# Optimization experiments

Measured on AMD Instinct MI355X. Metric: run time of the kernel, lower is better.

Reference implementation:

```python
import jax, jax.numpy as jnp
import numpy as np
from jax import lax

# Geometry constants (stand-in for beijing* globals)
A = 96           # beijingAngleNum
P = 4            # beijingPlanes
DET0, DET1 = 256, 8   # beijingSubDetectorSize [u, v]
NZ, NY, NX = 32, 256, 256  # beijingVolumeSize (nz = P * DET1)
T = 256          # ray integration steps
LAMB = 0.01


def _bilinear(vol, ix, iy):
    # vol: [nz, ny, nx]; ix, iy: [...] index-space coords. Zero outside.
    nz, ny, nx = vol.shape
    x0 = jnp.floor(ix); y0 = jnp.floor(iy)
    fx = (ix - x0).astype(vol.dtype); fy = (iy - y0).astype(vol.dtype)
    x0i = x0.astype(jnp.int32); y0i = y0.astype(jnp.int32)

    def g(yi, xi):
        valid = ((xi >= 0) & (xi < nx) & (yi >= 0) & (yi < ny)).astype(vol.dtype)
        v = vol[:, jnp.clip(yi, 0, ny - 1), jnp.clip(xi, 0, nx - 1)]  # [nz, ...]
        return v * valid

    return (g(y0i, x0i) * (1 - fy) * (1 - fx)
            + g(y0i, x0i + 1) * (1 - fy) * fx
            + g(y0i + 1, x0i) * fy * (1 - fx)
            + g(y0i + 1, x0i + 1) * fy * fx)


def forward_project(vol):
    # vol: [NZ, NY, NX] -> sinogram [A, NZ, DET0], parallel-beam over 180 deg
    angles = jnp.arange(A, dtype=jnp.float32) * (np.pi / A)
    u = jnp.arange(DET0, dtype=jnp.float32) - (DET0 - 1) / 2.0  # detector coord
    t = jnp.arange(T, dtype=jnp.float32) - (T - 1) / 2.0        # along-ray coord

    def per_angle(_, th):
        c, s = jnp.cos(th), jnp.sin(th)
        x = -u[:, None] * s + t[None, :] * c   # [DET0, T]
        y = u[:, None] * c + t[None, :] * s
        samp = _bilinear(vol, x + (NX - 1) / 2.0, y + (NY - 1) / 2.0)  # [NZ,DET0,T]
        return None, samp.sum(-1)  # line integral, [NZ, DET0]

    _, S = lax.scan(per_angle, None, angles)
    return S  # [A, NZ, DET0]


def back_project(S):
    # S: [A, NZ, DET0] -> volume [NZ, NY, NX] (adjoint-style backprojection)
    angles = jnp.arange(A, dtype=jnp.float32) * (np.pi / A)
    yy = jnp.arange(NY, dtype=jnp.float32) - (NY - 1) / 2.0
    xx = jnp.arange(NX, dtype=jnp.float32) - (NX - 1) / 2.0
    Y, X = jnp.meshgrid(yy, xx, indexing='ij')  # [NY, NX]

    def per_angle(acc, inp):
        th, Sa = inp  # Sa: [NZ, DET0]
        c, s = jnp.cos(th), jnp.sin(th)
        ub = -X * s + Y * c + (DET0 - 1) / 2.0  # detector bin coord [NY,NX]
        u0 = jnp.floor(ub)
        fu = (ub - u0).astype(Sa.dtype)
        u0i = u0.astype(jnp.int32)

        def g(ui):
            valid = ((ui >= 0) & (ui < DET0)).astype(Sa.dtype)
            return Sa[:, jnp.clip(ui, 0, DET0 - 1)] * valid  # [NZ,NY,NX]

        val = g(u0i) * (1 - fu) + g(u0i + 1) * fu
        return acc + val, None

    vol0 = jnp.zeros((NZ, NY, NX), dtype=S.dtype)
    vol, _ = lax.scan(per_angle, vol0, (angles, S))
    return vol


def setup_inputs() -> dict:
    key = jax.random.key(0)
    k1, k2 = jax.random.split(key)
    x = jax.random.normal(k1, (1, 1, NZ, NY, NX), dtype=jnp.float32)
    p = jax.random.normal(k2, (1, 1, A * P, DET1, DET0), dtype=jnp.float32)
    return {"x": x, "p": p}


def reference(x, p):
    vol = x[0, 0]                              # [NZ, NY, NX]
    S = forward_project(vol)                   # [A, NZ, DET0] native
    # ForwardProjection wrapper: (A,P,V,U) -> permute -> flat external layout
    ext = S.reshape(A, P, DET1, DET0).transpose(0, 2, 1, 3).reshape(1, 1, A * P, DET1, DET0)
    residual = ext - p
    # BackProjection wrapper: undo external layout back to native
    res_native = residual.reshape(A, DET1, P, DET0).transpose(0, 2, 1, 3).reshape(A, NZ, DET0)
    volb = back_project(res_native)            # [NZ, NY, NX]
    return (-LAMB * volb)[None, None]          # [1,1,NZ,NY,NX]
```

## Files before the change

kernel.cpp:

```cpp
#include <hip/hip_runtime.h>

#define A     96
#define DET0  256
#define NZ    32
#define NY    256
#define NX    256
#define T     256
#define LAMB  0.01f

#define TRIG_OFF  0
#define REST_OFF  256
#define VOLB_OFF  786688
#define PART_OFF  1835264
#define RES_ELEMS 786432

__device__ __forceinline__ unsigned short f2bf_rne(float f) {
    unsigned u = __float_as_uint(f);
    unsigned r = u + 0x7FFF + ((u >> 16) & 1);
    return (unsigned short)(r >> 16);
}
__device__ __forceinline__ float blo(unsigned u) { return __uint_as_float(u << 16); }
__device__ __forceinline__ float bhi(unsigned u) { return __uint_as_float(u & 0xFFFF0000u); }

__device__ __forceinline__ void acc8(float* acc, uint4 q, float w) {
    acc[0] = fmaf(w, blo(q.x), acc[0]); acc[1] = fmaf(w, bhi(q.x), acc[1]);
    acc[2] = fmaf(w, blo(q.y), acc[2]); acc[3] = fmaf(w, bhi(q.y), acc[3]);
    acc[4] = fmaf(w, blo(q.z), acc[4]); acc[5] = fmaf(w, bhi(q.z), acc[5]);
    acc[6] = fmaf(w, blo(q.w), acc[6]); acc[7] = fmaf(w, bhi(q.w), acc[7]);
}

__global__ __launch_bounds__(256) void k_transpose(const float* __restrict__ src,
                                                   unsigned short* __restrict__ vol_b,
                                                   float* __restrict__ trig) {
    __shared__ float lds[64 * 33];
    const int y   = blockIdx.y;
    const int x0  = blockIdx.x * 64;
    const int tid = threadIdx.x;

    if (blockIdx.x == 0 && y == 0 && tid < A) {
        float th = (float)tid * (float)(3.14159265358979323846 / (double)A);
        trig[2 * tid]     = cosf(th);
        trig[2 * tid + 1] = sinf(th);
    }

    const int xr = tid & 63;
    const int zr = tid >> 6;
    #pragma unroll
    for (int pz = 0; pz < 8; ++pz) {
        int z = pz * 4 + zr;
        lds[xr * 33 + z] = src[(z * NY + y) * NX + x0 + xr];
    }
    __syncthreads();
    const int zw = tid & 31;
    const int xw = tid >> 5;
    #pragma unroll
    for (int px = 0; px < 8; ++px) {
        int xi = px * 8 + xw;
        vol_b[(y * NX + x0 + xi) * NZ + zw] = f2bf_rne(lds[xi * 33 + zw]);
    }
}

__device__ __forceinline__ void rng(float g, float b, float L, float H,
                                    float& lo, float& hi) {
    if (fabsf(g) > 1e-5f) {
        float r0 = (L - b) / g, r1 = (H - b) / g;
        lo = fminf(r0, r1); hi = fmaxf(r0, r1);
    } else {
        bool in = (b >= L && b <= H);
        lo = in ? -1e9f : 1e9f;
        hi = in ? 1e9f : -1e9f;
    }
}
__device__ __forceinline__ int clampi(float v) {
    return (int)fminf(fmaxf(v, -2.f), 258.f);
}

__device__ __forceinline__ void sample_edge(const char* base, float ix, float iy,
                                            float* acc) {
    float xf = floorf(ix), yf = floorf(iy);
    float fx = ix - xf, fy = iy - yf;
    int x0 = (int)xf, y0 = (int)yf;
    float wx0 = 1.f - fx, wx1 = fx, wy0 = 1.f - fy, wy1 = fy;
    if ((unsigned)x0 >= NX)       wx0 = 0.f;
    if ((unsigned)(x0 + 1) >= NX) wx1 = 0.f;
    if ((unsigned)y0 >= NY)       wy0 = 0.f;
    if ((unsigned)(y0 + 1) >= NY) wy1 = 0.f;
    if ((wx0 == 0.f && wx1 == 0.f) || (wy0 == 0.f && wy1 == 0.f)) return;
    int cx0 = min(max(x0, 0), NX - 1);
    int cx1 = min(max(x0 + 1, 0), NX - 1);
    int cy0 = min(max(y0, 0), NY - 1);
    int cy1 = min(max(y0 + 1, 0), NY - 1);
    uint4 q00 = *(const uint4*)(base + ((size_t)((cy0 << 8) + cx0) << 6));
    uint4 q01 = *(const uint4*)(base + ((size_t)((cy0 << 8) + cx1) << 6));
    uint4 q10 = *(const uint4*)(base + ((size_t)((cy1 << 8) + cx0) << 6));
    uint4 q11 = *(const uint4*)(base + ((size_t)((cy1 << 8) + cx1) << 6));
    acc8(acc, q00, wy0 * wx0);
    acc8(acc, q01, wy0 * wx1);
    acc8(acc, q10, wy1 * wx0);
    acc8(acc, q11, wy1 * wx1);
}

__global__ __launch_bounds__(256) void k_forward(const unsigned short* __restrict__ vol_b,
                                                 const float* __restrict__ trig,
                                                 float* __restrict__ part,
                                                 int tlen) {
    const int tid = threadIdx.x;
    const int a  = blockIdx.z;
    const int u  = blockIdx.x * 64 + (tid >> 2);
    const int zq = tid & 3;
    const int t0 = blockIdx.y * tlen;

    const float c = trig[2 * a];
    const float s = trig[2 * a + 1];
    const float uu = (float)u - 127.5f;
    const float bx = fmaf(-uu, s, 127.5f);
    const float by = fmaf(uu, c, 127.5f);

    float lo1, hi1, lo2, hi2;
    rng(c, bx, -1.f, 256.f, lo1, hi1);
    rng(s, by, -1.f, 256.f, lo2, hi2);
    float fl = fmaxf(lo1, lo2), fh = fminf(hi1, hi2);
    int tF0 = max(t0, clampi(ceilf(fl + 127.5f)));
    int tF1 = min(t0 + tlen - 1, clampi(floorf(fh + 127.5f)));
    rng(c, bx, 1.f, 253.5f, lo1, hi1);
    rng(s, by, 1.f, 253.5f, lo2, hi2);
    float il = fmaxf(lo1, lo2), ih = fminf(hi1, hi2);
    int tI0 = max(clampi(ceilf(il + 127.5f)) + 1, tF0);
    int tI1 = min(clampi(floorf(ih + 127.5f)) - 1, tF1);
    if (tI0 > tI1) { tI0 = tF1 + 1; tI1 = tF1; }

    const char* base = (const char*)vol_b + zq * 16;
    float acc[8];
    #pragma unroll
    for (int k = 0; k < 8; ++k) acc[k] = 0.f;

    for (int t = tF0; t < tI0; ++t) {
        float ttf = (float)t - 127.5f;
        sample_edge(base, fmaf(ttf, c, bx), fmaf(ttf, s, by), acc);
    }
    for (int t = tI0; t <= tI1; ++t) {
        float ttf = (float)t - 127.5f;
        float ix = fmaf(ttf, c, bx);
        float iy = fmaf(ttf, s, by);
        float xf = floorf(ix), yf = floorf(iy);
        float fx = ix - xf, fy = iy - yf;
        int row = ((int)yf << 8) + (int)xf;
        const char* p0 = base + ((size_t)row << 6);
        uint4 q00 = *(const uint4*)(p0);
        uint4 q01 = *(const uint4*)(p0 + 64);
        uint4 q10 = *(const uint4*)(p0 + 16384);
        uint4 q11 = *(const uint4*)(p0 + 16384 + 64);
        float wx0 = 1.f - fx, wy0 = 1.f - fy;
        acc8(acc, q00, wy0 * wx0);
        acc8(acc, q01, wy0 * fx);
        acc8(acc, q10, fy * wx0);
        acc8(acc, q11, fy * fx);
    }
    for (int t = tI1 + 1; t <= tF1; ++t) {
        float ttf = (float)t - 127.5f;
        sample_edge(base, fmaf(ttf, c, bx), fmaf(ttf, s, by), acc);
    }

    float4* dst = (float4*)(part + (size_t)blockIdx.y * RES_ELEMS +
                            ((a * DET0 + u) * NZ + zq * 8));
    dst[0] = make_float4(acc[0], acc[1], acc[2], acc[3]);
    dst[1] = make_float4(acc[4], acc[5], acc[6], acc[7]);
}

__global__ __launch_bounds__(256) void k_combine(const float* __restrict__ p,
                                                 const float* __restrict__ part,
                                                 float* __restrict__ res_t,
                                                 int C) {
    __shared__ float lds[256 * 33];
    const int a = blockIdx.x;
    const int u = threadIdx.x;
    #pragma unroll
    for (int z = 0; z < 32; ++z) {
        int pidx = a * 8192 + (((z & 7) << 2) + (z >> 3)) * 256 + u;
        lds[u * 33 + z] = p[pidx];
    }
    __syncthreads();
    #pragma unroll
    for (int k = 0; k < 8; ++k) {
        int j4 = k * 256 + threadIdx.x;
        int j  = j4 * 4;
        int uu = j >> 5;
        int zb = j & 31;
        float4 v = make_float4(-lds[uu * 33 + zb],     -lds[uu * 33 + zb + 1],
                               -lds[uu * 33 + zb + 2], -lds[uu * 33 + zb + 3]);
        for (int c = 0; c < C; ++c) {
            float4 w = ((const float4*)(part + (size_t)c * RES_ELEMS))[a * 2048 + j4];
            v.x += w.x; v.y += w.y; v.z += w.z; v.w += w.w;
        }
        ((float4*)res_t)[a * 2048 + j4] = v;
    }
}

__global__ __launch_bounds__(256) void k_backward(const float* __restrict__ res_t,
                                                  const float* __restrict__ trig,
                                                  float* __restrict__ out) {
    __shared__ float4 wb[A * 32];
    __shared__ float  ob[32 * 33];
    const int tid = threadIdx.x;
    const int y  = blockIdx.y;
    const int xb = blockIdx.x * 32;

    for (int e = tid; e < A * 32; e += 256) {
        int a  = e >> 5;
        int xs = e & 31;
        float cc = trig[2 * a];
        float ss = trig[2 * a + 1];
        float xx = (float)(xb + xs) - 127.5f;
        float yy = (float)y - 127.5f;
        float ub = fmaf(-xx, ss, fmaf(yy, cc, 127.5f));
        float uf = floorf(ub);
        float fu = ub - uf;
        int i0 = (int)uf;
        float w0 = ((unsigned)i0 < DET0) ? (1.f - fu) : 0.f;
        float w1 = ((unsigned)(i0 + 1) < DET0) ? fu : 0.f;
        int c0 = min(max(i0, 0), DET0 - 1);
        int c1 = min(max(i0 + 1, 0), DET0 - 1);
        wb[e] = make_float4(w0, w1,
                            __int_as_float(((a * DET0 + c0) * NZ) << 2),
                            __int_as_float(((a * DET0 + c1) * NZ) << 2));
    }
    __syncthreads();

    const int xs = tid >> 3;
    const int zq = tid & 7;
    const char* rbase = (const char*)res_t + zq * 16;
    float4 acc = make_float4(0.f, 0.f, 0.f, 0.f);
    #pragma unroll 4
    for (int a = 0; a < A; ++a) {
        float4 e = wb[a * 32 + xs];
        float4 v0 = *(const float4*)(rbase + __float_as_int(e.z));
        float4 v1 = *(const float4*)(rbase + __float_as_int(e.w));
        acc.x = fmaf(e.x, v0.x, fmaf(e.y, v1.x, acc.x));
        acc.y = fmaf(e.x, v0.y, fmaf(e.y, v1.y, acc.y));
        acc.z = fmaf(e.x, v0.z, fmaf(e.y, v1.z, acc.z));
        acc.w = fmaf(e.x, v0.w, fmaf(e.y, v1.w, acc.w));
    }

    ob[(zq * 4 + 0) * 33 + xs] = acc.x;
    ob[(zq * 4 + 1) * 33 + xs] = acc.y;
    ob[(zq * 4 + 2) * 33 + xs] = acc.z;
    ob[(zq * 4 + 3) * 33 + xs] = acc.w;
    __syncthreads();

    const int z  = tid >> 3;
    const int x4 = (tid & 7) * 4;
    float4 o = make_float4(ob[z * 33 + x4],     ob[z * 33 + x4 + 1],
                           ob[z * 33 + x4 + 2], ob[z * 33 + x4 + 3]);
    float4* dst = (float4*)(out + (size_t)z * (NY * NX) + y * NX + xb + x4);
    *dst = make_float4(-LAMB * o.x, -LAMB * o.y, -LAMB * o.z, -LAMB * o.w);
}

extern "C" void kernel_launch(void* const* d_in, const int* in_sizes, int n_in,
                              void* d_out, int out_size, void* d_ws, size_t ws_size,
                              hipStream_t stream) {
    const float* x = (const float*)d_in[0];
    const float* p = (const float*)d_in[1];
    float* out = (float*)d_out;
    float* ws  = (float*)d_ws;

    float*          trig  = ws + TRIG_OFF;
    float*          res_t = ws + REST_OFF;
    unsigned short* vol_b = (unsigned short*)(ws + VOLB_OFF);
    float*          part  = ws + PART_OFF;

    size_t avail = ws_size / 4;
    int C = 8;
    while (C > 1 && (size_t)PART_OFF + (size_t)C * RES_ELEMS > avail) C >>= 1;
    int tlen = T / C;

    k_transpose<<<dim3(NX / 64, NY), 256, 0, stream>>>(x, vol_b, trig);
    k_forward  <<<dim3(4, C, A), 256, 0, stream>>>(vol_b, trig, part, tlen);
    k_combine  <<<dim3(A), 256, 0, stream>>>(p, part, res_t, C);
    k_backward <<<dim3(NX / 32, NY), 256, 0, stream>>>(res_t, trig, out);
}
```

Before: 205.4 us.

## Use fp32 volume, balance forward ray chunks, register-block backprojection rows

The forward volume copy is now stored in fp32 instead of bf16. This drops the bf16 rounding but doubles the bytes each bilinear gather reads. The forward kernel cuts rays into 32-step windows paired from both ends, spreads them over 4 partials to balance load, and uses a 1D grid ordered by angle with launch_bounds(256,4). The combine kernel runs on more blocks, and the backward kernel drops the LDS weight table in favour of computing weights inline, with each thread now covering 4 y rows to reuse trig and cut launch overhead.

```diff
diff --git a/kernel.cpp b/kernel.cpp
--- a/kernel.cpp
+++ b/kernel.cpp
@@ -10,27 +10,12 @@
 
 #define TRIG_OFF  0
 #define REST_OFF  256
-#define VOLB_OFF  786688
-#define PART_OFF  1835264
+#define VOLT_OFF  786688
+#define PART_OFF  2883840
 #define RES_ELEMS 786432
 
-__device__ __forceinline__ unsigned short f2bf_rne(float f) {
-    unsigned u = __float_as_uint(f);
-    unsigned r = u + 0x7FFF + ((u >> 16) & 1);
-    return (unsigned short)(r >> 16);
-}
-__device__ __forceinline__ float blo(unsigned u) { return __uint_as_float(u << 16); }
-__device__ __forceinline__ float bhi(unsigned u) { return __uint_as_float(u & 0xFFFF0000u); }
-
-__device__ __forceinline__ void acc8(float* acc, uint4 q, float w) {
-    acc[0] = fmaf(w, blo(q.x), acc[0]); acc[1] = fmaf(w, bhi(q.x), acc[1]);
-    acc[2] = fmaf(w, blo(q.y), acc[2]); acc[3] = fmaf(w, bhi(q.y), acc[3]);
-    acc[4] = fmaf(w, blo(q.z), acc[4]); acc[5] = fmaf(w, bhi(q.z), acc[5]);
-    acc[6] = fmaf(w, blo(q.w), acc[6]); acc[7] = fmaf(w, bhi(q.w), acc[7]);
-}
-
 __global__ __launch_bounds__(256) void k_transpose(const float* __restrict__ src,
-                                                   unsigned short* __restrict__ vol_b,
+                                                   float* __restrict__ vol_t,
                                                    float* __restrict__ trig) {
     __shared__ float lds[64 * 33];
     const int y   = blockIdx.y;
@@ -56,8 +41,15 @@
     #pragma unroll
     for (int px = 0; px < 8; ++px) {
         int xi = px * 8 + xw;
-        vol_b[(y * NX + x0 + xi) * NZ + zw] = f2bf_rne(lds[xi * 33 + zw]);
-    }
+        vol_t[(size_t)(y * NX + x0 + xi) * NZ + zw] = lds[xi * 33 + zw];
+    }
+}
+
+__device__ __forceinline__ void acc8f(float* acc, float4 qa, float4 qb, float w) {
+    acc[0] = fmaf(w, qa.x, acc[0]); acc[1] = fmaf(w, qa.y, acc[1]);
+    acc[2] = fmaf(w, qa.z, acc[2]); acc[3] = fmaf(w, qa.w, acc[3]);
+    acc[4] = fmaf(w, qb.x, acc[4]); acc[5] = fmaf(w, qb.y, acc[5]);
+    acc[6] = fmaf(w, qb.z, acc[6]); acc[7] = fmaf(w, qb.w, acc[7]);
 }
 
 __device__ __forceinline__ void rng(float g, float b, float L, float H,
@@ -90,25 +82,28 @@
     int cx1 = min(max(x0 + 1, 0), NX - 1);
     int cy0 = min(max(y0, 0), NY - 1);
     int cy1 = min(max(y0 + 1, 0), NY - 1);
-    uint4 q00 = *(const uint4*)(base + ((size_t)((cy0 << 8) + cx0) << 6));
-    uint4 q01 = *(const uint4*)(base + ((size_t)((cy0 << 8) + cx1) << 6));
-    uint4 q10 = *(const uint4*)(base + ((size_t)((cy1 << 8) + cx0) << 6));
-    uint4 q11 = *(const uint4*)(base + ((size_t)((cy1 << 8) + cx1) << 6));
-    acc8(acc, q00, wy0 * wx0);
-    acc8(acc, q01, wy0 * wx1);
-    acc8(acc, q10, wy1 * wx0);
-    acc8(acc, q11, wy1 * wx1);
-}
-
-__global__ __launch_bounds__(256) void k_forward(const unsigned short* __restrict__ vol_b,
-                                                 const float* __restrict__ trig,
-                                                 float* __restrict__ part,
-                                                 int tlen) {
-    const int tid = threadIdx.x;
-    const int a  = blockIdx.z;
-    const int u  = blockIdx.x * 64 + (tid >> 2);
+    const char* p00 = base + ((size_t)((cy0 << 8) + cx0) << 7);
+    const char* p01 = base + ((size_t)((cy0 << 8) + cx1) << 7);
+    const char* p10 = base + ((size_t)((cy1 << 8) + cx0) << 7);
+    const char* p11 = base + ((size_t)((cy1 << 8) + cx1) << 7);
+    acc8f(acc, *(const float4*)p00, *(const float4*)(p00 + 16), wy0 * wx0);
+    acc8f(acc, *(const float4*)p01, *(const float4*)(p01 + 16), wy0 * wx1);
+    acc8f(acc, *(const float4*)p10, *(const float4*)(p10 + 16), wy1 * wx0);
+    acc8f(acc, *(const float4*)p11, *(const float4*)(p11 + 16), wy1 * wx1);
+}
+
+__global__ __launch_bounds__(256, 4) void k_forward(const float* __restrict__ vol_t,
+                                                    const float* __restrict__ trig,
+                                                    float* __restrict__ part,
+                                                    int P) {
+    const unsigned bid = blockIdx.x;
+    const unsigned a   = bid % (unsigned)A;
+    const unsigned r   = bid / (unsigned)A;
+    const unsigned pr  = r % (unsigned)P;
+    const unsigned ug  = r / (unsigned)P;
+    const int tid = threadIdx.x;
+    const int u  = ug * 64 + (tid >> 2);
     const int zq = tid & 3;
-    const int t0 = blockIdx.y * tlen;
 
     const float c = trig[2 * a];
     const float s = trig[2 * a + 1];
@@ -120,49 +115,64 @@
     rng(c, bx, -1.f, 256.f, lo1, hi1);
     rng(s, by, -1.f, 256.f, lo2, hi2);
     float fl = fmaxf(lo1, lo2), fh = fminf(hi1, hi2);
-    int tF0 = max(t0, clampi(ceilf(fl + 127.5f)));
-    int tF1 = min(t0 + tlen - 1, clampi(floorf(fh + 127.5f)));
+    const int gF0 = clampi(ceilf(fl + 127.5f));
+    const int gF1 = clampi(floorf(fh + 127.5f));
     rng(c, bx, 1.f, 253.5f, lo1, hi1);
     rng(s, by, 1.f, 253.5f, lo2, hi2);
     float il = fmaxf(lo1, lo2), ih = fminf(hi1, hi2);
-    int tI0 = max(clampi(ceilf(il + 127.5f)) + 1, tF0);
-    int tI1 = min(clampi(floorf(ih + 127.5f)) - 1, tF1);
-    if (tI0 > tI1) { tI0 = tF1 + 1; tI1 = tF1; }
-
-    const char* base = (const char*)vol_b + zq * 16;
+    const int gI0 = clampi(ceilf(il + 127.5f)) + 1;
+    const int gI1 = clampi(floorf(ih + 127.5f)) - 1;
+
+    const char* base = (const char*)vol_t + zq * 32;
     float acc[8];
     #pragma unroll
     for (int k = 0; k < 8; ++k) acc[k] = 0.f;
 
-    for (int t = tF0; t < tI0; ++t) {
-        float ttf = (float)t - 127.5f;
-        sample_edge(base, fmaf(ttf, c, bx), fmaf(ttf, s, by), acc);
-    }
-    for (int t = tI0; t <= tI1; ++t) {
-        float ttf = (float)t - 127.5f;
-        float ix = fmaf(ttf, c, bx);
-        float iy = fmaf(ttf, s, by);
-        float xf = floorf(ix), yf = floorf(iy);
-        float fx = ix - xf, fy = iy - yf;
-        int row = ((int)yf << 8) + (int)xf;
-        const char* p0 = base + ((size_t)row << 6);
-        uint4 q00 = *(const uint4*)(p0);
-        uint4 q01 = *(const uint4*)(p0 + 64);
-        uint4 q10 = *(const uint4*)(p0 + 16384);
-        uint4 q11 = *(const uint4*)(p0 + 16384 + 64);
-        float wx0 = 1.f - fx, wy0 = 1.f - fy;
-        acc8(acc, q00, wy0 * wx0);
-        acc8(acc, q01, wy0 * fx);
-        acc8(acc, q10, fy * wx0);
-        acc8(acc, q11, fy * fx);
-    }
-    for (int t = tI1 + 1; t <= tF1; ++t) {
-        float ttf = (float)t - 127.5f;
-        sample_edge(base, fmaf(ttf, c, bx), fmaf(ttf, s, by), acc);
-    }
-
-    float4* dst = (float4*)(part + (size_t)blockIdx.y * RES_ELEMS +
-                            ((a * DET0 + u) * NZ + zq * 8));
+    for (int wi = (int)pr; wi < 4; wi += P) {
+        #pragma unroll
+        for (int side = 0; side < 2; ++side) {
+            int w = side ? (7 - wi) : wi;
+            int tF0 = max(w * 32, gF0);
+            int tF1 = min(w * 32 + 31, gF1);
+            int tI0 = max(gI0, tF0);
+            int tI1 = min(gI1, tF1);
+            if (tI0 > tI1) { tI0 = tF1 + 1; tI1 = tF1; }
+
+            for (int t = tF0; t < tI0; ++t) {
+                float ttf = (float)t - 127.5f;
+                sample_edge(base, fmaf(ttf, c, bx), fmaf(ttf, s, by), acc);
+            }
+            for (int t = tI0; t <= tI1; ++t) {
+                float ttf = (float)t - 127.5f;
+                float ix = fmaf(ttf, c, bx);
+                float iy = fmaf(ttf, s, by);
+                float xf = floorf(ix), yf = floorf(iy);
+                float fx = ix - xf, fy = iy - yf;
+                int row = ((int)yf << 8) + (int)xf;
+                const char* p0 = base + ((size_t)row << 7);
+                float4 a00 = *(const float4*)(p0);
+                float4 b00 = *(const float4*)(p0 + 16);
+                float4 a01 = *(const float4*)(p0 + 128);
+                float4 b01 = *(const float4*)(p0 + 144);
+                float4 a10 = *(const float4*)(p0 + 32768);
+                float4 b10 = *(const float4*)(p0 + 32784);
+                float4 a11 = *(const float4*)(p0 + 32896);
+                float4 b11 = *(const float4*)(p0 + 32912);
+                float wx0 = 1.f - fx, wy0 = 1.f - fy;
+                acc8f(acc, a00, b00, wy0 * wx0);
+                acc8f(acc, a01, b01, wy0 * fx);
+                acc8f(acc, a10, b10, fy * wx0);
+                acc8f(acc, a11, b11, fy * fx);
+            }
+            for (int t = tI1 + 1; t <= tF1; ++t) {
+                float ttf = (float)t - 127.5f;
+                sample_edge(base, fmaf(ttf, c, bx), fmaf(ttf, s, by), acc);
+            }
+        }
+    }
+
+    float4* dst = (float4*)(part + (size_t)pr * RES_ELEMS +
+                            (((int)a * DET0 + u) * NZ + zq * 8));
     dst[0] = make_float4(acc[0], acc[1], acc[2], acc[3]);
     dst[1] = make_float4(acc[4], acc[5], acc[6], acc[7]);
 }
@@ -170,89 +180,92 @@
 __global__ __launch_bounds__(256) void k_combine(const float* __restrict__ p,
                                                  const float* __restrict__ part,
                                                  float* __restrict__ res_t,
-                                                 int C) {
-    __shared__ float lds[256 * 33];
-    const int a = blockIdx.x;
-    const int u = threadIdx.x;
-    #pragma unroll
-    for (int z = 0; z < 32; ++z) {
-        int pidx = a * 8192 + (((z & 7) << 2) + (z >> 3)) * 256 + u;
-        lds[u * 33 + z] = p[pidx];
+                                                 int P) {
+    __shared__ float lds[64 * 33];
+    const int a  = blockIdx.x;
+    const int uq = blockIdx.y;
+    const int tid = threadIdx.x;
+    #pragma unroll
+    for (int k = 0; k < 8; ++k) {
+        int e  = k * 256 + tid;
+        int uo = e & 63;
+        int z  = e >> 6;
+        int pidx = a * 8192 + (((z & 7) << 2) + (z >> 3)) * 256 + uq * 64 + uo;
+        lds[uo * 33 + z] = p[pidx];
     }
     __syncthreads();
     #pragma unroll
-    for (int k = 0; k < 8; ++k) {
-        int j4 = k * 256 + threadIdx.x;
-        int j  = j4 * 4;
-        int uu = j >> 5;
-        int zb = j & 31;
-        float4 v = make_float4(-lds[uu * 33 + zb],     -lds[uu * 33 + zb + 1],
-                               -lds[uu * 33 + zb + 2], -lds[uu * 33 + zb + 3]);
-        for (int c = 0; c < C; ++c) {
-            float4 w = ((const float4*)(part + (size_t)c * RES_ELEMS))[a * 2048 + j4];
+    for (int k = 0; k < 2; ++k) {
+        int j4 = k * 256 + tid;
+        int uo = j4 >> 3;
+        int zb = (j4 & 7) * 4;
+        float4 v = make_float4(-lds[uo * 33 + zb],     -lds[uo * 33 + zb + 1],
+                               -lds[uo * 33 + zb + 2], -lds[uo * 33 + zb + 3]);
+        size_t gi = (size_t)a * 2048 + uq * 512 + j4;
+        for (int c = 0; c < P; ++c) {
+            float4 w = ((const float4*)(part + (size_t)c * RES_ELEMS))[gi];
             v.x += w.x; v.y += w.y; v.z += w.z; v.w += w.w;
         }
-        ((float4*)res_t)[a * 2048 + j4] = v;
+        ((float4*)res_t)[gi] = v;
     }
 }
 
 __global__ __launch_bounds__(256) void k_backward(const float* __restrict__ res_t,
                                                   const float* __restrict__ trig,
                                                   float* __restrict__ out) {
-    __shared__ float4 wb[A * 32];
-    __shared__ float  ob[32 * 33];
-    const int tid = threadIdx.x;
-    const int y  = blockIdx.y;
+    __shared__ float ob[32 * 33];
+    const int tid = threadIdx.x;
+    const int xs = tid >> 3;
+    const int zq = tid & 7;
     const int xb = blockIdx.x * 32;
-
-    for (int e = tid; e < A * 32; e += 256) {
-        int a  = e >> 5;
-        int xs = e & 31;
+    const int yb = blockIdx.y * 4;
+    const float xx = (float)(xb + xs) - 127.5f;
+    const float yy = (float)yb - 127.5f;
+
+    float4 acc[4];
+    #pragma unroll
+    for (int k = 0; k < 4; ++k) acc[k] = make_float4(0.f, 0.f, 0.f, 0.f);
+
+    const char* rbase = (const char*)res_t + zq * 16;
+    for (int a = 0; a < A; ++a) {
         float cc = trig[2 * a];
         float ss = trig[2 * a + 1];
-        float xx = (float)(xb + xs) - 127.5f;
-        float yy = (float)y - 127.5f;
         float ub = fmaf(-xx, ss, fmaf(yy, cc, 127.5f));
-        float uf = floorf(ub);
-        float fu = ub - uf;
-        int i0 = (int)uf;
-        float w0 = ((unsigned)i0 < DET0) ? (1.f - fu) : 0.f;
-        float w1 = ((unsigned)(i0 + 1) < DET0) ? fu : 0.f;
-        int c0 = min(max(i0, 0), DET0 - 1);
-        int c1 = min(max(i0 + 1, 0), DET0 - 1);
-        wb[e] = make_float4(w0, w1,
-                            __int_as_float(((a * DET0 + c0) * NZ) << 2),
-                            __int_as_float(((a * DET0 + c1) * NZ) << 2));
-    }
-    __syncthreads();
-
-    const int xs = tid >> 3;
-    const int zq = tid & 7;
-    const char* rbase = (const char*)res_t + zq * 16;
-    float4 acc = make_float4(0.f, 0.f, 0.f, 0.f);
-    #pragma unroll 4
-    for (int a = 0; a < A; ++a) {
-        float4 e = wb[a * 32 + xs];
-        float4 v0 = *(const float4*)(rbase + __float_as_int(e.z));
-        float4 v1 = *(const float4*)(rbase + __float_as_int(e.w));
-        acc.x = fmaf(e.x, v0.x, fmaf(e.y, v1.x, acc.x));
-        acc.y = fmaf(e.x, v0.y, fmaf(e.y, v1.y, acc.y));
-        acc.z = fmaf(e.x, v0.z, fmaf(e.y, v1.z, acc.z));
-        acc.w = fmaf(e.x, v0.w, fmaf(e.y, v1.w, acc.w));
-    }
-
-    ob[(zq * 4 + 0) * 33 + xs] = acc.x;
-    ob[(zq * 4 + 1) * 33 + xs] = acc.y;
-    ob[(zq * 4 + 2) * 33 + xs] = acc.z;
-    ob[(zq * 4 + 3) * 33 + xs] = acc.w;
-    __syncthreads();
-
-    const int z  = tid >> 3;
-    const int x4 = (tid & 7) * 4;
-    float4 o = make_float4(ob[z * 33 + x4],     ob[z * 33 + x4 + 1],
-                           ob[z * 33 + x4 + 2], ob[z * 33 + x4 + 3]);
-    float4* dst = (float4*)(out + (size_t)z * (NY * NX) + y * NX + xb + x4);
-    *dst = make_float4(-LAMB * o.x, -LAMB * o.y, -LAMB * o.z, -LAMB * o.w);
+        int abase = a * DET0;
+        #pragma unroll
+        for (int y = 0; y < 4; ++y) {
+            float uf = floorf(ub);
+            float fu = ub - uf;
+            int i0 = (int)uf;
+            float w0 = ((unsigned)i0 < 256u) ? (1.f - fu) : 0.f;
+            float w1 = ((unsigned)(i0 + 1) < 256u) ? fu : 0.f;
+            int c0 = min(max(i0, 0), 255);
+            int c1 = min(max(i0 + 1, 0), 255);
+            float4 v0 = *(const float4*)(rbase + ((size_t)(abase + c0) << 7));
+            float4 v1 = *(const float4*)(rbase + ((size_t)(abase + c1) << 7));
+            acc[y].x = fmaf(w0, v0.x, fmaf(w1, v1.x, acc[y].x));
+            acc[y].y = fmaf(w0, v0.y, fmaf(w1, v1.y, acc[y].y));
+            acc[y].z = fmaf(w0, v0.z, fmaf(w1, v1.z, acc[y].z));
+            acc[y].w = fmaf(w0, v0.w, fmaf(w1, v1.w, acc[y].w));
+            ub += cc;
+        }
+    }
+
+    #pragma unroll
+    for (int y = 0; y < 4; ++y) {
+        __syncthreads();
+        ob[(zq * 4 + 0) * 33 + xs] = acc[y].x;
+        ob[(zq * 4 + 1) * 33 + xs] = acc[y].y;
+        ob[(zq * 4 + 2) * 33 + xs] = acc[y].z;
+        ob[(zq * 4 + 3) * 33 + xs] = acc[y].w;
+        __syncthreads();
+        int z  = tid >> 3;
+        int x4 = (tid & 7) * 4;
+        float4 o = make_float4(ob[z * 33 + x4],     ob[z * 33 + x4 + 1],
+                               ob[z * 33 + x4 + 2], ob[z * 33 + x4 + 3]);
+        *(float4*)(out + (size_t)z * (NY * NX) + (yb + y) * NX + xb + x4) =
+            make_float4(-LAMB * o.x, -LAMB * o.y, -LAMB * o.z, -LAMB * o.w);
+    }
 }
 
 extern "C" void kernel_launch(void* const* d_in, const int* in_sizes, int n_in,
@@ -263,18 +276,17 @@
     float* out = (float*)d_out;
     float* ws  = (float*)d_ws;
 
-    float*          trig  = ws + TRIG_OFF;
-    float*          res_t = ws + REST_OFF;
-    unsigned short* vol_b = (unsigned short*)(ws + VOLB_OFF);
-    float*          part  = ws + PART_OFF;
+    float* trig  = ws + TRIG_OFF;
+    float* res_t = ws + REST_OFF;
+    float* vol_t = ws + VOLT_OFF;
+    float* part  = ws + PART_OFF;
 
     size_t avail = ws_size / 4;
-    int C = 8;
-    while (C > 1 && (size_t)PART_OFF + (size_t)C * RES_ELEMS > avail) C >>= 1;
-    int tlen = T / C;
-
-    k_transpose<<<dim3(NX / 64, NY), 256, 0, stream>>>(x, vol_b, trig);
-    k_forward  <<<dim3(4, C, A), 256, 0, stream>>>(vol_b, trig, part, tlen);
-    k_combine  <<<dim3(A), 256, 0, stream>>>(p, part, res_t, C);
-    k_backward <<<dim3(NX / 32, NY), 256, 0, stream>>>(res_t, trig, out);
-}
+    int P = 4;
+    while (P > 1 && (size_t)PART_OFF + (size_t)P * RES_ELEMS > avail) P >>= 1;
+
+    k_transpose<<<dim3(NX / 64, NY), 256, 0, stream>>>(x, vol_t, trig);
+    k_forward  <<<dim3(4 * P * A), 256, 0, stream>>>(vol_t, trig, part, P);
+    k_combine  <<<dim3(A, 4), 256, 0, stream>>>(p, part, res_t, P);
+    k_backward <<<dim3(NX / 32, NY / 4), 256, 0, stream>>>(res_t, trig, out);
+}
```

Result: slower. 259.6 us (+26.4%).
